# Performance work log

Hardware: AMD Instinct MI355X
Metric: run time of the kernel (lower is better)

## Reference

```python
import jax, jax.numpy as jnp
import numpy as np

CHAMFER_W, NORMAL_W, EDGE_W, WATERTIGHT_W, SDF_W = 1.0, 0.5, 0.3, 0.2, 1.0
DIHEDRAL_THRESHOLD = 0.5
EPS_COS = 1e-8   # F.cosine_similarity eps
EPS_NRM = 1e-12  # F.normalize eps


def _pairwise_sqdist(p, g):
    # (B,N,3),(B,M,3) -> (B,N,M) squared distances, without (B,N,M,3) temp
    p2 = (p * p).sum(-1)
    g2 = (g * g).sum(-1)
    return p2[:, :, None] + g2[:, None, :] - 2.0 * jnp.einsum('bnd,bmd->bnm', p, g)


def _face_normals(verts, faces):
    v0, v1, v2 = verts[faces[:, 0]], verts[faces[:, 1]], verts[faces[:, 2]]
    n = jnp.cross(v1 - v0, v2 - v0)
    return n / jnp.maximum(jnp.linalg.norm(n, axis=-1, keepdims=True), EPS_NRM)


def _edge_structure(faces, num_verts):
    # All 3F directed edges (f_i, f_{(i+1)%3}), canonicalized to sorted keys.
    a = faces                      # (F,3)
    b = jnp.roll(faces, -1, axis=1)  # pairs (0,1),(1,2),(2,0)
    lo = jnp.minimum(a, b).reshape(-1)
    hi = jnp.maximum(a, b).reshape(-1)
    keys = lo * num_verts + hi      # unique int key per undirected edge (< 2^31)
    face_ids = jnp.repeat(jnp.arange(faces.shape[0], dtype=jnp.int32), 3)
    order = jnp.argsort(keys, stable=True)
    sk = keys[order]
    sf = face_ids[order]
    E = sk.shape[0]
    run_start = jnp.concatenate([jnp.array([True]), sk[1:] != sk[:-1]])
    eq_next = jnp.concatenate([sk[:-1] == sk[1:], jnp.array([False])])
    rs_pad = jnp.concatenate([run_start, jnp.array([True, True])])
    # pair2[i]: run of length exactly 2 starting at i -> faces sf[i], sf[i+1]
    pair2 = run_start & eq_next & rs_pad[2:]
    return sf, pair2, run_start


def _edge_sharpness(verts, faces):
    normals = _face_normals(verts, faces)
    sf, pair2, _ = _edge_structure(faces, verts.shape[0])
    sf_next = jnp.roll(sf, -1)
    cos = (normals[sf] * normals[sf_next]).sum(-1)
    terms = jax.nn.relu(cos - DIHEDRAL_THRESHOLD)
    cnt = pair2.sum()
    return jnp.where(cnt > 0, (terms * pair2).sum() / jnp.maximum(cnt, 1), 0.0)


def _watertight(faces, num_verts):
    _, pair2, run_start = _edge_structure(faces, num_verts)
    total = run_start.sum()
    bad = total - pair2.sum()
    return jnp.where(total > 0, bad.astype(jnp.float32) / jnp.maximum(total, 1).astype(jnp.float32), 0.0)


def setup_inputs():
    key = jax.random.key(0)
    ks = jax.random.split(key, 10)
    B, N, M, V, F, NS = 1, 8192, 8192, 20000, 40000, 65536
    return {
        'pred_sdf': jax.random.normal(ks[0], (B, NS, 1), jnp.float32),
        'gt_sdf': jax.random.normal(ks[1], (B, NS, 1), jnp.float32),
        'extracted_vertices': jax.random.normal(ks[2], (V, 3), jnp.float32),
        'extracted_faces': jax.random.randint(ks[3], (F, 3), 0, V, jnp.int32),
        'gt_vertices': jax.random.normal(ks[4], (V, 3), jnp.float32),
        'gt_faces': jax.random.randint(ks[5], (F, 3), 0, V, jnp.int32),
        'pred_points': jax.random.normal(ks[6], (B, N, 3), jnp.float32),
        'gt_points': jax.random.normal(ks[7], (B, M, 3), jnp.float32),
        'pred_normals': jax.random.normal(ks[8], (B, N, 3), jnp.float32),
        'gt_normals': jax.random.normal(ks[9], (B, M, 3), jnp.float32),
    }


def reference(pred_sdf, gt_sdf, extracted_vertices, extracted_faces, gt_vertices, gt_faces,
              pred_points, gt_points, pred_normals, gt_normals):
    # sdf supervision (L1)
    sdf_l = SDF_W * jnp.abs(pred_sdf - gt_sdf).mean()

    # chamfer
    dist = _pairwise_sqdist(pred_points, gt_points)  # (B,N,M)
    min_p2g = dist.min(axis=2).mean(axis=1)
    min_g2p = dist.min(axis=1).mean(axis=1)
    chamfer_l = CHAMFER_W * (min_p2g + min_g2p).mean()

    # normal consistency (nearest GT point per pred point)
    nn_idx = jnp.argmin(dist, axis=2)  # (B,N)
    matched = jnp.take_along_axis(gt_normals, nn_idx[..., None], axis=1)  # (B,N,3)
    pn = jnp.maximum(jnp.linalg.norm(pred_normals, axis=-1), EPS_COS)
    gn = jnp.maximum(jnp.linalg.norm(matched, axis=-1), EPS_COS)
    cos = (pred_normals * matched).sum(-1) / (pn * gn)
    normal_l = NORMAL_W * (1.0 - jnp.abs(cos)).mean()

    # edge sharpness (GT mesh args are unused by the original implementation)
    edge_l = EDGE_W * _edge_sharpness(extracted_vertices, extracted_faces)

    # watertight regularization
    wt_l = WATERTIGHT_W * _watertight(extracted_faces, extracted_vertices.shape[0])

    total = sdf_l + chamfer_l + normal_l + edge_l + wt_l
    return sdf_l, chamfer_l, normal_l, edge_l, wt_l, total
```

## Files before the change

### kernel.cpp

```cpp
#include <hip/hip_runtime.h>
#include <math.h>

#define TILE 128
#define REG 4
#define APB (256 * REG)
#define HASH_C 262144
#define HASH_MASK (HASH_C - 1)
#define KEY_MASK ((1u << 29) - 1)
#define CNT_ONE (1u << 29)


__device__ inline unsigned f2sortable(float f) {
  unsigned b = __float_as_uint(f);
  return (b & 0x80000000u) ? ~b : (b | 0x80000000u);
}
__device__ inline float sortable2f(unsigned u) {
  unsigned b = (u & 0x80000000u) ? (u ^ 0x80000000u) : ~u;
  return __uint_as_float(b);
}
__device__ inline float waveReduceF(float v) {
#pragma unroll
  for (int off = 32; off > 0; off >>= 1) v += __shfl_down(v, off, 64);
  return v;
}

__global__ __launch_bounds__(256) void mesh_prep_kernel(
    const float* __restrict__ verts, const int* __restrict__ faces, int F, int V,
    int N, int M, float4* __restrict__ fn, unsigned* __restrict__ slots,
    unsigned* __restrict__ face0, unsigned* __restrict__ face1,
    unsigned long long* __restrict__ p2g, unsigned* __restrict__ g2p) {
  int e = blockIdx.x * 256 + threadIdx.x;
  if (e < N) p2g[e] = ~0ull;
  if (e < M) g2p[e] = ~0u;
  if (e >= 3 * F) return;
  int f = e / 3, k = e - 3 * f;
  int a = faces[3 * f + k];
  int b = faces[3 * f + ((k + 1) % 3)];
  if (k == 0) {
    int i1 = faces[3 * f + 1], i2 = faces[3 * f + 2];
    float ax = verts[3 * a], ay = verts[3 * a + 1], az = verts[3 * a + 2];
    float bx = verts[3 * i1] - ax, by = verts[3 * i1 + 1] - ay, bz = verts[3 * i1 + 2] - az;
    float cx = verts[3 * i2] - ax, cy = verts[3 * i2 + 1] - ay, cz = verts[3 * i2 + 2] - az;
    float nx = by * cz - bz * cy;
    float ny = bz * cx - bx * cz;
    float nz = bx * cy - by * cx;
    float l = sqrtf(nx * nx + ny * ny + nz * nz);
    float inv = 1.f / fmaxf(l, 1e-12f);
    fn[f] = make_float4(nx * inv, ny * inv, nz * inv, 0.f);
  }
  unsigned lo = (unsigned)min(a, b), hi = (unsigned)max(a, b);
  unsigned key = lo * (unsigned)V + hi + 1u;
  unsigned h = (key * 2654435761u) & HASH_MASK;
  unsigned c;
  for (;;) {
    unsigned prev = atomicCAS(&slots[h], 0u, key | CNT_ONE);
    if (prev == 0u) { c = 0u; break; }
    if ((prev & KEY_MASK) == key) {
      c = (atomicAdd(&slots[h], CNT_ONE) >> 29) & 7u;
      break;
    }
    h = (h + 1) & HASH_MASK;
  }
  if (c == 0u) face0[h] = (unsigned)f;
  else if (c == 1u) face1[h] = (unsigned)f;
}

__global__ __launch_bounds__(256) void chamfer_kernel(
    const float* __restrict__ P, const float* __restrict__ G, int N, int M,
    int p2gBlocks, int nTileG, int nTileP,
    unsigned long long* __restrict__ p2g, unsigned* __restrict__ g2p) {
  __shared__ float4 tile[TILE];
  int tid = threadIdx.x;
  bool isP2G = (blockIdx.x < p2gBlocks);
  const float* A;
  const float* B;
  int nA, nB, chunk, tileIdx;
  if (isP2G) {
    chunk = blockIdx.x / nTileG;
    tileIdx = blockIdx.x % nTileG;
    A = P; nA = N; B = G; nB = M;
  } else {
    int bid = blockIdx.x - p2gBlocks;
    chunk = bid / nTileP;
    tileIdx = bid % nTileP;
    A = G; nA = M; B = P; nB = N;
  }

  int abase = chunk * APB + tid;
  float px[REG], py[REG], pz[REG], best[REG];
  int bi[REG];
#pragma unroll
  for (int r = 0; r < REG; r++) {
    int i = abase + 256 * r;
    if (i < nA) { px[r] = A[3 * i]; py[r] = A[3 * i + 1]; pz[r] = A[3 * i + 2]; }
    else        { px[r] = 0.f; py[r] = 0.f; pz[r] = 0.f; }
    best[r] = INFINITY;
    bi[r] = 0;
  }

  int tbase = tileIdx * TILE;
  if (tid < TILE) {
    int j = tbase + tid;
    float4 v;
    if (j < nB) {
      float x = B[3 * j], y = B[3 * j + 1], z = B[3 * j + 2];
      v = make_float4(x, y, z, 0.5f * (x * x + y * y + z * z));
    } else {
      v = make_float4(0.f, 0.f, 0.f, INFINITY);
    }
    tile[tid] = v;
  }
  __syncthreads();

  if (isP2G) {
#pragma unroll 2
    for (int j = 0; j < TILE; j += 2) {
      float4 g0 = tile[j];
      float4 g1 = tile[j + 1];
#pragma unroll
      for (int r = 0; r < REG; r++) {
        float s0 = fmaf(-pz[r], g0.z, fmaf(-py[r], g0.y, fmaf(-px[r], g0.x, g0.w)));
        float s1 = fmaf(-pz[r], g1.z, fmaf(-py[r], g1.y, fmaf(-px[r], g1.x, g1.w)));
        float sm = (s1 < s0) ? s1 : s0;
        int im = (s1 < s0) ? (j + 1) : j;
        if (sm < best[r]) { best[r] = sm; bi[r] = im; }
      }
    }
#pragma unroll
    for (int r = 0; r < REG; r++) {
      int i = abase + 256 * r;
      if (i < nA) {
        unsigned long long packed =
            ((unsigned long long)f2sortable(best[r]) << 32) |
            (unsigned)(tbase + bi[r]);
        atomicMin(&p2g[i], packed);
      }
    }
  } else {
#pragma unroll 2
    for (int j = 0; j < TILE; j += 2) {
      float4 g0 = tile[j];
      float4 g1 = tile[j + 1];
#pragma unroll
      for (int r = 0; r < REG; r++) {
        float s0 = fmaf(-pz[r], g0.z, fmaf(-py[r], g0.y, fmaf(-px[r], g0.x, g0.w)));
        float s1 = fmaf(-pz[r], g1.z, fmaf(-py[r], g1.y, fmaf(-px[r], g1.x, g1.w)));
        best[r] = fminf(best[r], fminf(s0, s1));
      }
    }
#pragma unroll
    for (int r = 0; r < REG; r++) {
      int i = abase + 256 * r;
      if (i < nA) atomicMin(&g2p[i], f2sortable(best[r]));
    }
  }
}

__global__ __launch_bounds__(256) void finalize_kernel(
    const float* __restrict__ P, const float* __restrict__ G,
    const float* __restrict__ PN, const float* __restrict__ GN,
    const float* __restrict__ sdfA, const float* __restrict__ sdfB,
    const unsigned* __restrict__ slots, const unsigned* __restrict__ face0,
    const unsigned* __restrict__ face1, const float4* __restrict__ fn,
    int N, int M, int NS, int nBlocks,
    const unsigned long long* __restrict__ p2g, const unsigned* __restrict__ g2p,
    float* accumF, unsigned* accumU, float* out) {
  __shared__ float sh[28];
  int t = blockIdx.x * 256 + threadIdx.x;
  int stride = nBlocks * 256;
  float sp = 0.f, sg = 0.f, sn = 0.f, ss = 0.f, term = 0.f;
  unsigned runs = 0, pairs = 0;
  if (t < N) {
    unsigned long long pk = p2g[t];
    float s = sortable2f((unsigned)(pk >> 32));
    int idx = (int)(pk & 0xFFFFFFFFull);
    float px = P[3 * t], py = P[3 * t + 1], pz = P[3 * t + 2];
    sp = px * px + py * py + pz * pz + 2.f * s;
    float nx = PN[3 * t], ny = PN[3 * t + 1], nz = PN[3 * t + 2];
    float mx = GN[3 * idx], my = GN[3 * idx + 1], mz = GN[3 * idx + 2];
    float pn = fmaxf(sqrtf(nx * nx + ny * ny + nz * nz), 1e-8f);
    float gn = fmaxf(sqrtf(mx * mx + my * my + mz * mz), 1e-8f);
    float cosv = (nx * mx + ny * my + nz * mz) / (pn * gn);
    sn = 1.f - fabsf(cosv);
  }
  if (t < M) {
    float s = sortable2f(g2p[t]);
    float gx = G[3 * t], gy = G[3 * t + 1], gz = G[3 * t + 2];
    sg = gx * gx + gy * gy + gz * gz + 2.f * s;
  }
  for (int i = t; i < NS; i += stride) ss += fabsf(sdfA[i] - sdfB[i]);
  for (int h = t; h < HASH_C; h += stride) {
    unsigned s = slots[h];
    if (s != 0u) {
      runs++;
      if ((s >> 29) == 2u) {
        pairs++;
        float4 n0 = fn[face0[h]];
        float4 n1 = fn[face1[h]];
        float c = n0.x * n1.x + n0.y * n1.y + n0.z * n1.z;
        term += fmaxf(c - 0.5f, 0.f);
      }
    }
  }
  sp = waveReduceF(sp);
  sg = waveReduceF(sg);
  sn = waveReduceF(sn);
  ss = waveReduceF(ss);
  term = waveReduceF(term);
  float fruns = waveReduceF((float)runs);
  float fpairs = waveReduceF((float)pairs);
  int lane = threadIdx.x & 63, wid = threadIdx.x >> 6;
  if (lane == 0) {
    sh[wid] = sp; sh[4 + wid] = sg; sh[8 + wid] = sn; sh[12 + wid] = ss;
    sh[16 + wid] = term; sh[20 + wid] = fruns; sh[24 + wid] = fpairs;
  }
  __syncthreads();
  if (threadIdx.x == 0) {
    atomicAdd(&accumF[1], sh[0] + sh[1] + sh[2] + sh[3]);
    atomicAdd(&accumF[2], sh[4] + sh[5] + sh[6] + sh[7]);
    atomicAdd(&accumF[3], sh[8] + sh[9] + sh[10] + sh[11]);
    atomicAdd(&accumF[0], sh[12] + sh[13] + sh[14] + sh[15]);
    atomicAdd(&accumF[4], sh[16] + sh[17] + sh[18] + sh[19]);
    atomicAdd(&accumF[5], sh[20] + sh[21] + sh[22] + sh[23]);
    atomicAdd(&accumF[6], sh[24] + sh[25] + sh[26] + sh[27]);
    __threadfence();
    unsigned ticket = atomicAdd(&accumU[0], 1u);
    if (ticket == (unsigned)(nBlocks - 1)) {
      float a0 = atomicAdd(&accumF[0], 0.f);
      float a1 = atomicAdd(&accumF[1], 0.f);
      float a2 = atomicAdd(&accumF[2], 0.f);
      float a3 = atomicAdd(&accumF[3], 0.f);
      float a4 = atomicAdd(&accumF[4], 0.f);
      float runsF = atomicAdd(&accumF[5], 0.f);
      float pairsF = atomicAdd(&accumF[6], 0.f);
      float sdf = a0 / (float)NS;
      float chamfer = a1 / (float)N + a2 / (float)M;
      float normal = 0.5f * (a3 / (float)N);
      float edge = (pairsF > 0.f) ? 0.3f * (a4 / pairsF) : 0.f;
      float wt = (runsF > 0.f) ? 0.2f * ((runsF - pairsF) / runsF) : 0.f;
      out[0] = sdf;
      out[1] = chamfer;
      out[2] = normal;
      out[3] = edge;
      out[4] = wt;
      out[5] = sdf + chamfer + normal + edge + wt;
    }
  }
}

extern "C" void kernel_launch(void* const* d_in, const int* in_sizes, int n_in,
                              void* d_out, int out_size, void* d_ws,
                              size_t ws_size, hipStream_t stream) {
  const float* pred_sdf = (const float*)d_in[0];
  const float* gt_sdf   = (const float*)d_in[1];
  const float* ev       = (const float*)d_in[2];
  const int*   ef       = (const int*)d_in[3];
  const float* pp       = (const float*)d_in[6];
  const float* gp       = (const float*)d_in[7];
  const float* pn       = (const float*)d_in[8];
  const float* gn       = (const float*)d_in[9];
  int NS = in_sizes[0];
  int V = in_sizes[2] / 3;
  int F = in_sizes[3] / 3;
  int N = in_sizes[6] / 3;
  int M = in_sizes[7] / 3;
  float* out = (float*)d_out;

  char* ws = (char*)d_ws;
  size_t offSlots = 0;
  size_t offAccumF = offSlots + (size_t)HASH_C * 4;
  size_t offAccumU = offAccumF + 32;
  size_t zeroBytes = offAccumU + 32;
  size_t offP2G = (zeroBytes + 15) & ~(size_t)15;
  size_t offG2P = offP2G + (size_t)N * 8;
  size_t offFace0 = offG2P + (size_t)M * 4;
  size_t offFace1 = offFace0 + (size_t)HASH_C * 4;
  size_t offFN = (offFace1 + (size_t)HASH_C * 4 + 15) & ~(size_t)15;

  unsigned* slots = (unsigned*)(ws + offSlots);
  float* accumF = (float*)(ws + offAccumF);
  unsigned* accumU = (unsigned*)(ws + offAccumU);
  unsigned long long* p2gArr = (unsigned long long*)(ws + offP2G);
  unsigned* g2pArr = (unsigned*)(ws + offG2P);
  unsigned* face0 = (unsigned*)(ws + offFace0);
  unsigned* face1 = (unsigned*)(ws + offFace1);
  float4* fnorm = (float4*)(ws + offFN);

  hipMemsetAsync(ws + offSlots, 0, zeroBytes, stream);

  mesh_prep_kernel<<<(3 * F + 255) / 256, 256, 0, stream>>>(
      ev, ef, F, V, N, M, fnorm, slots, face0, face1, p2gArr, g2pArr);

  int nChunkP = (N + APB - 1) / APB, nTileG = (M + TILE - 1) / TILE;
  int nChunkG = (M + APB - 1) / APB, nTileP = (N + TILE - 1) / TILE;
  int p2gBlocks = nChunkP * nTileG;
  int g2pBlocks = nChunkG * nTileP;
  chamfer_kernel<<<p2gBlocks + g2pBlocks, 256, 0, stream>>>(
      pp, gp, N, M, p2gBlocks, nTileG, nTileP, p2gArr, g2pArr);

  int mx = (N > M ? N : M);
  int nFin = (mx + 255) / 256;
  if (nFin < 128) nFin = 128;
  finalize_kernel<<<nFin, 256, 0, stream>>>(
      pp, gp, pn, gn, pred_sdf, gt_sdf, slots, face0, face1, fnorm,
      N, M, NS, nFin, p2gArr, g2pArr, accumF, accumU, out);
}
```

Measured before the change: 127.6 us.

## Fuse mesh prep into chamfer kernel, memset NN arrays, raise per-thread register tile

Merges the mesh-preparation work (face normals, edge hash insertion) into the chamfer kernel as extra trailing blocks, so both run concurrently in one launch. The nearest-neighbour arrays are now initialised with a 0xFF memset instead of inside the prep kernel. Each thread also handles 8 query points instead of 4, which halves the number of chamfer blocks but raises register use. The aim is to cut one kernel launch and overlap the atomic-heavy hashing with the distance computation, at the cost of an extra memset and possibly lower occupancy.

```diff
diff --git a/kernel.cpp b/kernel.cpp
--- a/kernel.cpp
+++ b/kernel.cpp
@@ -2,7 +2,7 @@
 #include <math.h>
 
 #define TILE 128
-#define REG 4
+#define REG 8
 #define APB (256 * REG)
 #define HASH_C 262144
 #define HASH_MASK (HASH_C - 1)
@@ -24,54 +24,53 @@
   return v;
 }
 
-__global__ __launch_bounds__(256) void mesh_prep_kernel(
+__global__ __launch_bounds__(256) void fused_kernel(
+    const float* __restrict__ P, const float* __restrict__ G, int N, int M,
+    int p2gBlocks, int chamferBlocks, int nTileG, int nTileP,
+    unsigned long long* __restrict__ p2g, unsigned* __restrict__ g2p,
     const float* __restrict__ verts, const int* __restrict__ faces, int F, int V,
-    int N, int M, float4* __restrict__ fn, unsigned* __restrict__ slots,
-    unsigned* __restrict__ face0, unsigned* __restrict__ face1,
-    unsigned long long* __restrict__ p2g, unsigned* __restrict__ g2p) {
-  int e = blockIdx.x * 256 + threadIdx.x;
-  if (e < N) p2g[e] = ~0ull;
-  if (e < M) g2p[e] = ~0u;
-  if (e >= 3 * F) return;
-  int f = e / 3, k = e - 3 * f;
-  int a = faces[3 * f + k];
-  int b = faces[3 * f + ((k + 1) % 3)];
-  if (k == 0) {
-    int i1 = faces[3 * f + 1], i2 = faces[3 * f + 2];
-    float ax = verts[3 * a], ay = verts[3 * a + 1], az = verts[3 * a + 2];
-    float bx = verts[3 * i1] - ax, by = verts[3 * i1 + 1] - ay, bz = verts[3 * i1 + 2] - az;
-    float cx = verts[3 * i2] - ax, cy = verts[3 * i2 + 1] - ay, cz = verts[3 * i2 + 2] - az;
-    float nx = by * cz - bz * cy;
-    float ny = bz * cx - bx * cz;
-    float nz = bx * cy - by * cx;
-    float l = sqrtf(nx * nx + ny * ny + nz * nz);
-    float inv = 1.f / fmaxf(l, 1e-12f);
-    fn[f] = make_float4(nx * inv, ny * inv, nz * inv, 0.f);
-  }
-  unsigned lo = (unsigned)min(a, b), hi = (unsigned)max(a, b);
-  unsigned key = lo * (unsigned)V + hi + 1u;
-  unsigned h = (key * 2654435761u) & HASH_MASK;
-  unsigned c;
-  for (;;) {
-    unsigned prev = atomicCAS(&slots[h], 0u, key | CNT_ONE);
-    if (prev == 0u) { c = 0u; break; }
-    if ((prev & KEY_MASK) == key) {
-      c = (atomicAdd(&slots[h], CNT_ONE) >> 29) & 7u;
-      break;
-    }
-    h = (h + 1) & HASH_MASK;
-  }
-  if (c == 0u) face0[h] = (unsigned)f;
-  else if (c == 1u) face1[h] = (unsigned)f;
-}
-
-__global__ __launch_bounds__(256) void chamfer_kernel(
-    const float* __restrict__ P, const float* __restrict__ G, int N, int M,
-    int p2gBlocks, int nTileG, int nTileP,
-    unsigned long long* __restrict__ p2g, unsigned* __restrict__ g2p) {
+    float4* __restrict__ fn, unsigned* __restrict__ slots,
+    unsigned* __restrict__ face0, unsigned* __restrict__ face1) {
   __shared__ float4 tile[TILE];
   int tid = threadIdx.x;
-  bool isP2G = (blockIdx.x < p2gBlocks);
+
+  if (blockIdx.x >= (unsigned)chamferBlocks) {
+    int e = (blockIdx.x - chamferBlocks) * 256 + tid;
+    if (e >= 3 * F) return;
+    int f = e / 3, k = e - 3 * f;
+    int a = faces[3 * f + k];
+    int b = faces[3 * f + ((k + 1) % 3)];
+    if (k == 0) {
+      int i1 = faces[3 * f + 1], i2 = faces[3 * f + 2];
+      float ax = verts[3 * a], ay = verts[3 * a + 1], az = verts[3 * a + 2];
+      float bx = verts[3 * i1] - ax, by = verts[3 * i1 + 1] - ay, bz = verts[3 * i1 + 2] - az;
+      float cx = verts[3 * i2] - ax, cy = verts[3 * i2 + 1] - ay, cz = verts[3 * i2 + 2] - az;
+      float nx = by * cz - bz * cy;
+      float ny = bz * cx - bx * cz;
+      float nz = bx * cy - by * cx;
+      float l = sqrtf(nx * nx + ny * ny + nz * nz);
+      float inv = 1.f / fmaxf(l, 1e-12f);
+      fn[f] = make_float4(nx * inv, ny * inv, nz * inv, 0.f);
+    }
+    unsigned lo = (unsigned)min(a, b), hi = (unsigned)max(a, b);
+    unsigned key = lo * (unsigned)V + hi + 1u;
+    unsigned h = (key * 2654435761u) & HASH_MASK;
+    unsigned c;
+    for (;;) {
+      unsigned prev = atomicCAS(&slots[h], 0u, key | CNT_ONE);
+      if (prev == 0u) { c = 0u; break; }
+      if ((prev & KEY_MASK) == key) {
+        c = (atomicAdd(&slots[h], CNT_ONE) >> 29) & 7u;
+        break;
+      }
+      h = (h + 1) & HASH_MASK;
+    }
+    if (c == 0u) face0[h] = (unsigned)f;
+    else if (c == 1u) face1[h] = (unsigned)f;
+    return;
+  }
+
+  bool isP2G = ((int)blockIdx.x < p2gBlocks);
   const float* A;
   const float* B;
   int nA, nB, chunk, tileIdx;
@@ -273,7 +272,9 @@
   size_t zeroBytes = offAccumU + 32;
   size_t offP2G = (zeroBytes + 15) & ~(size_t)15;
   size_t offG2P = offP2G + (size_t)N * 8;
-  size_t offFace0 = offG2P + (size_t)M * 4;
+  size_t endFF = offG2P + (size_t)M * 4;
+  size_t ffBytes = endFF - offP2G;
+  size_t offFace0 = endFF;
   size_t offFace1 = offFace0 + (size_t)HASH_C * 4;
   size_t offFN = (offFace1 + (size_t)HASH_C * 4 + 15) & ~(size_t)15;
 
@@ -287,16 +288,16 @@
   float4* fnorm = (float4*)(ws + offFN);
 
   hipMemsetAsync(ws + offSlots, 0, zeroBytes, stream);
-
-  mesh_prep_kernel<<<(3 * F + 255) / 256, 256, 0, stream>>>(
-      ev, ef, F, V, N, M, fnorm, slots, face0, face1, p2gArr, g2pArr);
+  hipMemsetAsync(ws + offP2G, 0xFF, ffBytes, stream);
 
   int nChunkP = (N + APB - 1) / APB, nTileG = (M + TILE - 1) / TILE;
   int nChunkG = (M + APB - 1) / APB, nTileP = (N + TILE - 1) / TILE;
   int p2gBlocks = nChunkP * nTileG;
-  int g2pBlocks = nChunkG * nTileP;
-  chamfer_kernel<<<p2gBlocks + g2pBlocks, 256, 0, stream>>>(
-      pp, gp, N, M, p2gBlocks, nTileG, nTileP, p2gArr, g2pArr);
+  int chamferBlocks = p2gBlocks + nChunkG * nTileP;
+  int meshBlocks = (3 * F + 255) / 256;
+  fused_kernel<<<chamferBlocks + meshBlocks, 256, 0, stream>>>(
+      pp, gp, N, M, p2gBlocks, chamferBlocks, nTileG, nTileP, p2gArr, g2pArr,
+      ev, ef, F, V, fnorm, slots, face0, face1);
 
   int mx = (N > M ? N : M);
   int nFin = (mx + 255) / 256;
```

Measured after the change: 120.9 us. 5.3% less time.
